# Performance work log

Measured on AMD Instinct MI355X. Metric: run time of the kernel, lower is better.

The kernel has to match this reference:

```python
import jax, jax.numpy as jnp
import numpy as np
from jax import lax

H = 8          # num_heads
LAM = 4.0      # lambda_scale
POOL = 8       # pool_ratio (effective, N % POOL == 0)
NS_ITERS = 5
NS_EPS = 1e-4
WHITE_EPS = 1e-5


def _lap_kernel(x, y):
    # x: [B,H,n,D], y: [B,H,m,D] -> exp(-||x_i - y_j||_1 / LAM): [B,H,n,m]
    l1 = jnp.sum(jnp.abs(x[:, :, :, None, :] - y[:, :, None, :, :]), axis=-1)
    return jnp.exp(-l1 / LAM)


def setup_inputs() -> dict:
    key = jax.random.key(0)
    ks = jax.random.split(key, 8)
    B, N, C = 2, 1024, 512
    s = 0.05  # weight scale for realistic magnitudes
    return {
        "x": jax.random.normal(ks[0], (B, N, C), jnp.float32),
        "attention_mask": jnp.ones((B, N), jnp.float32),
        "qkv_w": jax.random.normal(ks[1], (3 * C, C), jnp.float32) * s,
        "qkv_b": jax.random.normal(ks[2], (3 * C,), jnp.float32) * s,
        "proj_w": jax.random.normal(ks[3], (C, C), jnp.float32) * s,
        "proj_b": jax.random.normal(ks[4], (C,), jnp.float32) * s,
        "dwc_w": jax.random.normal(ks[5], (C, 1, 3), jnp.float32) * s,
        "dwc_b": jax.random.normal(ks[6], (C,), jnp.float32) * s,
    }


def reference(x, attention_mask, qkv_w, qkv_b, proj_w, proj_b, dwc_w, dwc_b):
    B, N, C = x.shape
    D = C // H
    tm = attention_mask                      # [B,N]
    mh = tm[:, None, :, None]                # [B,1,N,1] broadcast over heads

    qkv = (x @ qkv_w.T + qkv_b).reshape(B, N, 3, H, D).transpose(2, 0, 3, 1, 4)
    q, k, v = qkv[0] * mh, qkv[1] * mh, qkv[2] * mh   # [B,H,N,D]

    # NOTE: faithful to source: raw reshape of [B,N,H*D] into [B,C,N]
    v_sp = v.transpose(0, 2, 1, 3).reshape(B, C, N)
    q_sp = q.transpose(0, 2, 1, 3).reshape(B, C, N)
    k_sp = k.transpose(0, 2, 1, 3).reshape(B, C, N)

    # depthwise conv1d, kernel 3, padding 1
    v_local = lax.conv_general_dilated(
        v_sp, dwc_w, window_strides=(1,), padding=[(1, 1)],
        feature_group_count=C, dimension_numbers=("NCH", "OIH", "NCH")
    ) + dwc_b[None, :, None]
    v_local = v_local.transpose(0, 2, 1) * tm[:, :, None]   # [B,N,C]

    p = POOL
    m = N // p
    pm = tm.reshape(B, 1, m, p).mean(-1)                    # [B,1,m]
    pms = jnp.clip(pm, 1e-6)
    q_pool = (q_sp * tm[:, None, :]).reshape(B, C, m, p).mean(-1) / pms
    k_pool = (k_sp * tm[:, None, :]).reshape(B, C, m, p).mean(-1) / pms
    lmask = (pm > 0).astype(x.dtype)[:, 0, :]               # [B,m]

    q_l = q_pool.transpose(0, 2, 1).reshape(B, m, H, D).transpose(0, 2, 1, 3)
    k_l = k_pool.transpose(0, 2, 1).reshape(B, m, H, D).transpose(0, 2, 1, 3)

    W = _lap_kernel(q_l, k_l)                               # [B,H,m,m]
    pair = lmask[:, None, :, None] * lmask[:, None, None, :]
    I = jnp.eye(m, dtype=x.dtype)[None, None]
    W = W * pair + I * (1.0 - pair)

    # Newton-Schulz pseudo-inverse
    W_eps = W + NS_EPS * I
    fro = jnp.sqrt(jnp.sum(W_eps * W_eps, axis=(-2, -1), keepdims=True))
    X = (2.0 / (fro + 1e-8)) * jnp.swapaxes(W_eps, -2, -1)
    for _ in range(NS_ITERS):
        X = X @ (2.0 * I - W_eps @ X)
    W_inv = X

    la_mask = lmask[:, None, None, :]                        # [B,1,1,m]
    C_q = _lap_kernel(q, k_l) * la_mask                      # [B,H,N,m]
    C_k = _lap_kernel(k, q_l) * la_mask                      # [B,H,N,m]

    # batch-statistics whitening of C_q over dims (0,2)
    qmask = tm[:, None, :, None]                             # [B,1,N,1]
    valid = jnp.clip(jnp.sum(qmask, axis=(0, 2), keepdims=True), 1.0)
    mu = jnp.sum(C_q * qmask, axis=(0, 2), keepdims=True) / valid
    cen = (C_q - mu) * qmask
    var = jnp.sum(cen * cen, axis=(0, 2), keepdims=True) / valid
    C_q_norm = ((C_q - mu) / jnp.sqrt(var + WHITE_EPS)) * qmask

    context = W_inv @ (jnp.swapaxes(C_k, -2, -1) @ v)        # [B,H,m,D]
    ga = (C_q_norm @ context) * mh                           # [B,H,N,D]
    ga = ga.transpose(0, 2, 1, 3).reshape(B, N, C)

    out = (ga + v_local) @ proj_w.T + proj_b
    return out * tm[:, :, None]
```

## Files before the change

### kernel.cpp

```cpp
#include <hip/hip_runtime.h>
#include <hip/hip_bf16.h>
#include <hip/hip_fp16.h>

#define Hh 8
#define Bz 2
#define Nn 1024
#define Cc 512
#define Dd 64
#define Mm 128
#define NS_EPS 1e-4f
#define WHITE_EPS 1e-5f

__device__ __forceinline__ float h2f(__half v) { return __half2float(v); }
__device__ __forceinline__ __half f2h(float v) { return __float2half(v); }

typedef _Float16 half8 __attribute__((ext_vector_type(8)));
typedef float float4v __attribute__((ext_vector_type(4)));

__global__ __launch_bounds__(256) void qkv_gemm(
    const float* __restrict__ x, const float* __restrict__ w,
    const float* __restrict__ bias, const float* __restrict__ tm,
    __half* __restrict__ Q, __half* __restrict__ K, __half* __restrict__ V) {
  __shared__ _Float16 As[128 * 40];
  __shared__ _Float16 Bs[128 * 40];
// ... 90 lines not shown
    for (int i = 0; i < 8; ++i) {
      float t = tm[b * 1024 + 8 * j + i];
      pm += t;
      sq += Qs[d][8 * jl + i] * t;
      sk += Ks[d][8 * jl + i] * t;
    }
    pm *= 0.125f;
    float pms = fmaxf(pm, 1e-6f);
    size_t oi = ((size_t)bh * 128 + j) * 64 + d;
    QL[oi] = f2h(sq * 0.125f / pms);
    KL[oi] = f2h(sk * 0.125f / pms);
    if (h == 0 && d == 0) LM[b * 128 + j] = (pm > 0.f) ? 1.f : 0.f;
  }
}

__global__ __launch_bounds__(256) void wbuild_kernel(
    const __half* __restrict__ QL, const __half* __restrict__ KL,
    const float* __restrict__ LM, float* __restrict__ W) {
  int it = blockIdx.x;
  int bh = blockIdx.y;
  int b = bh >> 3;
  int i0 = it * 16;
  __shared__ __align__(16) float kls[128 * 68];
  __shared__ __align__(16) float qs[16 * 68];
  __shared__ float ps[16 * 132];
  int tid = threadIdx.x;
  for (int e = tid; e < 8192; e += 256)
    kls[(e >> 6) * 68 + (e & 63)] = h2f(KL[(size_t)bh * 8192 + e]);
  for (int e = tid; e < 1024; e += 256)
    qs[(e >> 6) * 68 + (e & 63)] =
        h2f(QL[(size_t)bh * 8192 + (size_t)(i0 + (e >> 6)) * 64 + (e & 63)]);
  __syncthreads();
  int jg = tid & 63, ng = tid >> 6;
  int j = jg * 2;
  const float4* kA = (const float4*)&kls[j * 68];
  const float4* kB = (const float4*)&kls[(j + 1) * 68];
  float sA[4] = {}, sB[4] = {};
#pragma unroll
  for (int i = 0; i < 16; ++i) {
    int dq = (i + jg) & 15;
    float4 ka = kA[dq];
    float4 kb = kB[dq];
#pragma unroll
    for (int r = 0; r < 4; ++r) {
      float4 qv = *(const float4*)&qs[(ng * 4 + r) * 68 + dq * 4];
      sA[r] += fabsf(qv.x - ka.x) + fabsf(qv.y - ka.y) + fabsf(qv.z - ka.z) + fabsf(qv.w - ka.w);
      sB[r] += fabsf(qv.x - kb.x) + fabsf(qv.y - kb.y) + fabsf(qv.z - kb.z) + fabsf(qv.w - kb.w);
    }
  }
  float lmA = LM[b * Mm + j], lmB = LM[b * Mm + j + 1];
#pragma unroll
  for (int r = 0; r < 4; ++r) {
    int i = i0 + ng * 4 + r;
    float lmi = LM[b * Mm + i];
    float prA = lmi * lmA, prB = lmi * lmB;
    float dA = (i == j) ? 1.f : 0.f;
    float dB = (i == j + 1) ? 1.f : 0.f;
    ps[(ng * 4 + r) * 132 + j] = expf(-sA[r] * 0.25f) * prA + dA * (1.f - prA) + dA * NS_EPS;
    ps[(ng * 4 + r) * 132 + j + 1] = expf(-sB[r] * 0.25f) * prB + dB * (1.f - prB) + dB * NS_EPS;
  }
  __syncthreads();
  for (int e = tid; e < 2048; e += 256)
    W[(size_t)bh * (Mm * Mm) + (size_t)(i0 + (e >> 7)) * 128 + (e & 127)] =
        ps[(e >> 7) * 132 + (e & 127)];
}

__global__ __launch_bounds__(256) void ns_solve(const float* __restrict__ Wg,
                                                float* __restrict__ Xout) {
  int bh = blockIdx.x;
  __shared__ _Float16 Ws[128 * 136];
  __shared__ _Float16 Xa[128 * 136];
  __shared__ _Float16 Xb[128 * 136];
  __shared__ _Float16 Tt[128 * 136];
  __shared__ float red[256];
  int tid = threadIdx.x;
  const float* Wb = Wg + (size_t)bh * 16384;
  float fro = 0.f;
  for (int e = tid; e < 16384; e += 256) {
    float wv = Wb[e];
    Ws[(e >> 7) * 136 + (e & 127)] = (_Float16)wv;
    fro += wv * wv;
  }
  red[tid] = fro;
  __syncthreads();
  for (int off = 128; off > 0; off >>= 1) {
    if (tid < off) red[tid] += red[tid + off];
    __syncthreads();
  }
  float scale = 2.f / (sqrtf(red[0]) + 1e-8f);
  for (int e = tid; e < 16384; e += 256) {
    int i = e >> 7, k = e & 127;
    Xa[i * 136 + k] = (_Float16)(scale * (float)Ws[k * 136 + i]);
    Xb[i * 136 + k] = (_Float16)(scale * (float)Ws[i * 136 + k]);
  }
  __syncthreads();
  int lane = tid & 63, wv_ = tid >> 6;
  int wm = (wv_ >> 1) * 64, wn = (wv_ & 1) * 64;
  int l15 = lane & 15, quad = lane >> 4;
  for (int it = 0; it < 5; ++it) {
    {
      float4v acc[4][4] = {};
#pragma unroll
      for (int kt = 0; kt < 4; ++kt) {
        half8 a[4], b[4];
#pragma unroll
        for (int mt = 0; mt < 4; ++mt)
          a[mt] = *(const half8*)&Ws[(wm + mt * 16 + l15) * 136 + kt * 32 + quad * 8];
#pragma unroll
        for (int nt = 0; nt < 4; ++nt)
          b[nt] = *(const half8*)&Xb[(wn + nt * 16 + l15) * 136 + kt * 32 + quad * 8];
#pragma unroll
        for (int mt = 0; mt < 4; ++mt)
#pragma unroll
          for (int nt = 0; nt < 4; ++nt)
            acc[mt][nt] =
                __builtin_amdgcn_mfma_f32_16x16x32_f16(a[mt], b[nt], acc[mt][nt], 0, 0, 0);
      }
#pragma unroll
      for (int mt = 0; mt < 4; ++mt)
#pragma unroll
        for (int r = 0; r < 4; ++r) {
          int i = wm + mt * 16 + quad * 4 + r;
#pragma unroll
          for (int nt = 0; nt < 4; ++nt) {
            int j = wn + nt * 16 + l15;
            Tt[j * 136 + i] = (_Float16)(((i == j) ? 2.f : 0.f) - acc[mt][nt][r]);
          }
        }
    }
    __syncthreads();
    {
      float4v acc[4][4] = {};
#pragma unroll
      for (int kt = 0; kt < 4; ++kt) {
        half8 a[4], b[4];
#pragma unroll
        for (int mt = 0; mt < 4; ++mt)
          a[mt] = *(const half8*)&Xa[(wm + mt * 16 + l15) * 136 + kt * 32 + quad * 8];
#pragma unroll
        for (int nt = 0; nt < 4; ++nt)
          b[nt] = *(const half8*)&Tt[(wn + nt * 16 + l15) * 136 + kt * 32 + quad * 8];
#pragma unroll
        for (int mt = 0; mt < 4; ++mt)
#pragma unroll
          for (int nt = 0; nt < 4; ++nt)
            acc[mt][nt] =
                __builtin_amdgcn_mfma_f32_16x16x32_f16(a[mt], b[nt], acc[mt][nt], 0, 0, 0);
      }
      __syncthreads();
#pragma unroll
      for (int mt = 0; mt < 4; ++mt)
#pragma unroll
        for (int r = 0; r < 4; ++r) {
          int i = wm + mt * 16 + quad * 4 + r;
#pragma unroll
          for (int nt = 0; nt < 4; ++nt) {
            int j = wn + nt * 16 + l15;
            _Float16 v = (_Float16)acc[mt][nt][r];
            Xa[i * 136 + j] = v;
            Xb[j * 136 + i] = v;
          }
        }
    }
    __syncthreads();
  }
  for (int e = tid; e < 16384; e += 256)
    Xout[(size_t)bh * 16384 + e] = (float)Xa[(e >> 7) * 136 + (e & 127)];
}

__global__ __launch_bounds__(256) void ktv_fused(
    const __half* __restrict__ K, const __half* __restrict__ QL,
    const float* __restrict__ LM, const __half* __restrict__ V,
    float* __restrict__ KTVp) {
  int jt = blockIdx.x;
  int bh = blockIdx.y;
  int nc = blockIdx.z;
  int b = bh >> 3, h = bh & 7;
  int j0 = jt * 32;
  __shared__ __align__(16) float qls[32 * 68];
  __shared__ __align__(16) float Ks[32 * 68];
  __shared__ __align__(16) float Vs[32 * 68];
  __shared__ float P[32 * 36];
  int tid = threadIdx.x;
  int sr = tid >> 3, sd8 = (tid & 7) * 8;
  {
    half8 q = *(const half8*)(QL + (size_t)bh * 8192 + (size_t)(j0 + sr) * 64 + sd8);
    float4 f0 = {(float)q[0], (float)q[1], (float)q[2], (float)q[3]};
    float4 f1 = {(float)q[4], (float)q[5], (float)q[6], (float)q[7]};
    *(float4*)&qls[sr * 68 + sd8] = f0;
    *(float4*)&qls[sr * 68 + sd8 + 4] = f1;
  }
  int jq = tid & 15, nq = tid >> 4;
  int dq2 = tid & 7, jl = tid >> 3;
  float acc[8] = {};
  for (int nt = 0; nt < 4; ++nt) {
    int n0 = nc * 128 + nt * 32;
    __syncthreads();
    {
      size_t gi = (size_t)b * (Nn * Cc) + (size_t)(n0 + sr) * 512 + h * 64 + sd8;
      half8 kv = *(const half8*)(K + gi);
      half8 vv = *(const half8*)(V + gi);
      float4 k0 = {(float)kv[0], (float)kv[1], (float)kv[2], (float)kv[3]};
      float4 k1 = {(float)kv[4], (float)kv[5], (float)kv[6], (float)kv[7]};
      float4 v0 = {(float)vv[0], (float)vv[1], (float)vv[2], (float)vv[3]};
      float4 v1 = {(float)vv[4], (float)vv[5], (float)vv[6], (float)vv[7]};
      *(float4*)&Ks[sr * 68 + sd8] = k0;
      *(float4*)&Ks[sr * 68 + sd8 + 4] = k1;
      *(float4*)&Vs[sr * 68 + sd8] = v0;
      *(float4*)&Vs[sr * 68 + sd8 + 4] = v1;
    }
    __syncthreads();
    {
      const float4* q0p = (const float4*)&qls[(jq * 2) * 68];
      const float4* q1p = (const float4*)&qls[(jq * 2 + 1) * 68];
      const float4* k0p = (const float4*)&Ks[(nq * 2) * 68];
      const float4* k1p = (const float4*)&Ks[(nq * 2 + 1) * 68];
      float s00 = 0.f, s01 = 0.f, s10 = 0.f, s11 = 0.f;
#pragma unroll
      for (int i = 0; i < 16; ++i) {
        int dq = (i + tid) & 15;
        float4 q0 = q0p[dq], q1 = q1p[dq];
        float4 k0 = k0p[dq], k1 = k1p[dq];
        s00 += fabsf(q0.x - k0.x) + fabsf(q0.y - k0.y) + fabsf(q0.z - k0.z) + fabsf(q0.w - k0.w);
        s01 += fabsf(q0.x - k1.x) + fabsf(q0.y - k1.y) + fabsf(q0.z - k1.z) + fabsf(q0.w - k1.w);
        s10 += fabsf(q1.x - k0.x) + fabsf(q1.y - k0.y) + fabsf(q1.z - k0.z) + fabsf(q1.w - k0.w);
        s11 += fabsf(q1.x - k1.x) + fabsf(q1.y - k1.y) + fabsf(q1.z - k1.z) + fabsf(q1.w - k1.w);
      }
      P[(nq * 2) * 36 + jq * 2] = expf(-s00 * 0.25f);
      P[(nq * 2) * 36 + jq * 2 + 1] = expf(-s10 * 0.25f);
      P[(nq * 2 + 1) * 36 + jq * 2] = expf(-s01 * 0.25f);
      P[(nq * 2 + 1) * 36 + jq * 2 + 1] = expf(-s11 * 0.25f);
    }
    __syncthreads();
    {
#pragma unroll 4
      for (int n = 0; n < 32; ++n) {
        float p = P[n * 36 + jl];
        float4 v0 = *(const float4*)&Vs[n * 68 + dq2 * 8];
        float4 v1 = *(const float4*)&Vs[n * 68 + dq2 * 8 + 4];
        acc[0] += p * v0.x; acc[1] += p * v0.y; acc[2] += p * v0.z; acc[3] += p * v0.w;
        acc[4] += p * v1.x; acc[5] += p * v1.y; acc[6] += p * v1.z; acc[7] += p * v1.w;
      }
    }
  }
  {
    float lm = LM[b * 128 + j0 + jl];
    float* dst = &KTVp[((size_t)nc * 16 + bh) * 8192 + (size_t)(j0 + jl) * 64 + dq2 * 8];
    float4 o0 = {acc[0] * lm, acc[1] * lm, acc[2] * lm, acc[3] * lm};
    float4 o1 = {acc[4] * lm, acc[5] * lm, acc[6] * lm, acc[7] * lm};
    *(float4*)dst = o0;
    *(float4*)(dst + 4) = o1;
  }
}

__global__ __launch_bounds__(256) void ctx_kernel(const float* __restrict__ X,
                                                  const float* __restrict__ KTVp,
                                                  __half* __restrict__ CTX) {
  int it = blockIdx.x;
  int bh = blockIdx.y;
  int i0 = it * 16;
  __shared__ __align__(16) float KTVs[8192];
  __shared__ float Xs[16][132];
  int tid = threadIdx.x;
  const float4* src = (const float4*)KTVp;
  for (int e = tid; e < 2048; e += 256) {
    float4 s = src[(size_t)bh * 2048 + e];
#pragma unroll
    for (int nc = 1; nc < 8; ++nc) {
      float4 v = src[((size_t)nc * 16 + bh) * 2048 + e];
      s.x += v.x; s.y += v.y; s.z += v.z; s.w += v.w;
    }
    *(float4*)&KTVs[e * 4] = s;
  }
  for (int e = tid; e < 2048; e += 256)
    Xs[e >> 7][e & 127] = X[(size_t)bh * 16384 + (size_t)(i0 + (e >> 7)) * 128 + (e & 127)];
  __syncthreads();
  int il = tid >> 4, dg = tid & 15;
  float a0 = 0.f, a1 = 0.f, a2 = 0.f, a3 = 0.f;
#pragma unroll 4
  for (int j = 0; j < 128; ++j) {
    float xv = Xs[il][j];
    float4 kv = *(const float4*)&KTVs[j * 64 + dg * 4];
    a0 += xv * kv.x; a1 += xv * kv.y; a2 += xv * kv.z; a3 += xv * kv.w;
  }
  size_t ob = (size_t)bh * 8192 + (size_t)(i0 + il) * 64 + dg * 4;
  CTX[ob] = f2h(a0);
  CTX[ob + 1] = f2h(a1);
  CTX[ob + 2] = f2h(a2);
  CTX[ob + 3] = f2h(a3);
}

__global__ __launch_bounds__(256) void stats_partial(
    const __half* __restrict__ Q, const __half* __restrict__ KL,
    const float* __restrict__ LM, const float* __restrict__ tm,
    float* __restrict__ PS, __half* __restrict__ Pbuf) {
  int jt = blockIdx.x;
  int bh = blockIdx.y;
  int nc = blockIdx.z;
  int b = bh >> 3, h = bh & 7;
  int j0 = jt * 32;
  __shared__ __align__(16) float kls[32 * 68];
  __shared__ __align__(16) float Qs[32 * 68];
  __shared__ float red[32 * 8 * 3];
  int tid = threadIdx.x;
  int sr = tid >> 3, sd8 = (tid & 7) * 8;
  {
    half8 q = *(const half8*)(KL + (size_t)bh * 8192 + (size_t)(j0 + sr) * 64 + sd8);
    float4 f0 = {(float)q[0], (float)q[1], (float)q[2], (float)q[3]};
    float4 f1 = {(float)q[4], (float)q[5], (float)q[6], (float)q[7]};
    *(float4*)&kls[sr * 68 + sd8] = f0;
    *(float4*)&kls[sr * 68 + sd8 + 4] = f1;
  }
  int jq = tid & 15, nq = tid >> 4;
  int jA = j0 + jq * 2, jB = jA + 1;
  float lmA = LM[b * 128 + jA], lmB = LM[b * 128 + jB];
  float aA1 = 0.f, aA2 = 0.f, aA3 = 0.f, aB1 = 0.f, aB2 = 0.f, aB3 = 0.f;
  for (int nt = 0; nt < 4; ++nt) {
    int n0 = nc * 128 + nt * 32;
    __syncthreads();
    {
      size_t gi = (size_t)b * (Nn * Cc) + (size_t)(n0 + sr) * 512 + h * 64 + sd8;
      half8 kv = *(const half8*)(Q + gi);
      float4 k0 = {(float)kv[0], (float)kv[1], (float)kv[2], (float)kv[3]};
      float4 k1 = {(float)kv[4], (float)kv[5], (float)kv[6], (float)kv[7]};
      *(float4*)&Qs[sr * 68 + sd8] = k0;
      *(float4*)&Qs[sr * 68 + sd8 + 4] = k1;
    }
    __syncthreads();
    const float4* q0p = (const float4*)&kls[(jq * 2) * 68];
    const float4* q1p = (const float4*)&kls[(jq * 2 + 1) * 68];
    const float4* k0p = (const float4*)&Qs[(nq * 2) * 68];
    const float4* k1p = (const float4*)&Qs[(nq * 2 + 1) * 68];
    float s00 = 0.f, s01 = 0.f, s10 = 0.f, s11 = 0.f;
#pragma unroll
    for (int i = 0; i < 16; ++i) {
      int dq = (i + tid) & 15;
      float4 q0 = q0p[dq], q1 = q1p[dq];
      float4 k0 = k0p[dq], k1 = k1p[dq];
      s00 += fabsf(q0.x - k0.x) + fabsf(q0.y - k0.y) + fabsf(q0.z - k0.z) + fabsf(q0.w - k0.w);
      s01 += fabsf(q0.x - k1.x) + fabsf(q0.y - k1.y) + fabsf(q0.z - k1.z) + fabsf(q0.w - k1.w);
      s10 += fabsf(q1.x - k0.x) + fabsf(q1.y - k0.y) + fabsf(q1.z - k0.z) + fabsf(q1.w - k0.w);
      s11 += fabsf(q1.x - k1.x) + fabsf(q1.y - k1.y) + fabsf(q1.z - k1.z) + fabsf(q1.w - k1.w);
    }
    int nA = n0 + nq * 2, nB = nA + 1;
    float tA = tm[b * 1024 + nA], tB = tm[b * 1024 + nB];
    float xAa = expf(-s00 * 0.25f) * lmA;
    float xAb = expf(-s01 * 0.25f) * lmA;
    float xBa = expf(-s10 * 0.25f) * lmB;
    float xBb = expf(-s11 * 0.25f) * lmB;
    Pbuf[((size_t)bh * 1024 + nA) * 128 + jA] = f2h(xAa);
    Pbuf[((size_t)bh * 1024 + nB) * 128 + jA] = f2h(xAb);
    Pbuf[((size_t)bh * 1024 + nA) * 128 + jB] = f2h(xBa);
    Pbuf[((size_t)bh * 1024 + nB) * 128 + jB] = f2h(xBb);
    float xt;
    xt = xAa * tA; aA1 += xt; aA2 += xt * xt; aA3 += xt * tA;
    xt = xAb * tB; aA1 += xt; aA2 += xt * xt; aA3 += xt * tB;
    xt = xBa * tA; aB1 += xt; aB2 += xt * xt; aB3 += xt * tA;
    xt = xBb * tB; aB1 += xt; aB2 += xt * xt; aB3 += xt * tB;
  }
  int jl = jq * 2;
  red[(jl * 8 + nq) * 3 + 0] = aA1;
  red[(jl * 8 + nq) * 3 + 1] = aA2;
  red[(jl * 8 + nq) * 3 + 2] = aA3;
  red[((jl + 1) * 8 + nq) * 3 + 0] = aB1;
  red[((jl + 1) * 8 + nq) * 3 + 1] = aB2;
  red[((jl + 1) * 8 + nq) * 3 + 2] = aB3;
  __syncthreads();
  if (tid < 32) {
    float s1 = 0.f, s2 = 0.f, s3 = 0.f;
#pragma unroll
    for (int q = 0; q < 8; ++q) {
      s1 += red[(tid * 8 + q) * 3 + 0];
      s2 += red[(tid * 8 + q) * 3 + 1];
      s3 += red[(tid * 8 + q) * 3 + 2];
    }
    size_t base = ((size_t)(nc * 16 + bh) * 128 + j0 + tid) * 3;
    PS[base] = s1; PS[base + 1] = s2; PS[base + 2] = s3;
  }
}

__global__ __launch_bounds__(256) void stats_final(const float* __restrict__ PS,
                                                   const float* __restrict__ tm,
                                                   float* __restrict__ MU,
                                                   float* __restrict__ RS) {
  __shared__ float red[256][2];
  __shared__ float ts0, ts1;
  int tid = threadIdx.x;
  float a = 0.f, c = 0.f;
  for (int i = tid; i < 2048; i += 256) { float t = tm[i]; a += t; c += t * t; }
  red[tid][0] = a; red[tid][1] = c;
  __syncthreads();
  for (int off = 128; off > 0; off >>= 1) {
    if (tid < off) { red[tid][0] += red[tid + off][0]; red[tid][1] += red[tid + off][1]; }
    __syncthreads();
  }
  if (tid == 0) { ts0 = red[0][0]; ts1 = red[0][1]; }
  __syncthreads();
  int hj = blockIdx.x * 256 + tid;
  int h = hj >> 7, j = hj & 127;
  float s1 = 0.f, s2 = 0.f, s3 = 0.f;
#pragma unroll
  for (int nc = 0; nc < 8; ++nc)
#pragma unroll
    for (int b = 0; b < 2; ++b) {
      const float* p = PS + ((size_t)(nc * 16 + b * 8 + h) * 128 + j) * 3;
      s1 += p[0]; s2 += p[1]; s3 += p[2];
    }
  float valid = fmaxf(ts0, 1.f);
  float mu = s1 / valid;
  float var = (s2 - 2.f * mu * s3 + mu * mu * ts1) / valid;
  var = fmaxf(var, 0.f);
  MU[hj] = mu;
  RS[hj] = rsqrtf(var + WHITE_EPS);
}

__global__ __launch_bounds__(256) void ga_fused(
    const __half* __restrict__ Pbuf, const float* __restrict__ MU,
    const float* __restrict__ RS, const __half* __restrict__ CTXg,
    const __half* __restrict__ V, const float* __restrict__ dwc_w,
    const float* __restrict__ dwc_b, const float* __restrict__ tm,
    __half* __restrict__ VL) {
  int bh = blockIdx.y;
  int b = bh >> 3, h = bh & 7;
  int n0 = blockIdx.x * 16;
  __shared__ __half Ps[16][130];
  __shared__ __align__(16) __half2 ctx2[128][32];
  __shared__ float musr[128][2];
  int tid = threadIdx.x;
// ... 106 lines not shown
                              void* d_out, int out_size, void* d_ws, size_t ws_size,
                              hipStream_t stream) {
  const float* x      = (const float*)d_in[0];
  const float* tm     = (const float*)d_in[1];
  const float* qkv_w  = (const float*)d_in[2];
  const float* qkv_b  = (const float*)d_in[3];
  const float* proj_w = (const float*)d_in[4];
  const float* proj_b = (const float*)d_in[5];
  const float* dwc_w  = (const float*)d_in[6];
  const float* dwc_b  = (const float*)d_in[7];
  float* out = (float*)d_out;

  char* wsb = (char*)d_ws;
  __half* Qh  = (__half*)(wsb + 0);
  __half* Kh  = (__half*)(wsb + 2097152);
  __half* Vh  = (__half*)(wsb + 4194304);
  __half* VLh = (__half*)(wsb + 6291456);
  __half* QLh = (__half*)(wsb + 8388608);
  __half* KLh = (__half*)(wsb + 8650752);
  float*  LM  = (float*)(wsb + 8912896);
  float*  MU  = (float*)(wsb + 8913920);
  float*  RS  = (float*)(wsb + 8918016);
  __half* CTX = (__half*)(wsb + 9446400);
  float*  XA  = (float*)(wsb + 9708544);
  float*  PS  = (float*)(wsb + 9708544 + 1048576);

  char* ob = (char*)d_out;
  float*  Wf   = (float*)ob;
  float*  KTVp = (float*)ob;
  __half* Pbuf = (__half*)ob;

  qkv_gemm<<<dim3(16, 12), 256, 0, stream>>>(x, qkv_w, qkv_b, tm, Qh, Kh, Vh);
  pool_kernel<<<dim3(16, 16), 256, 0, stream>>>(Qh, Kh, tm, QLh, KLh, LM);
  wbuild_kernel<<<dim3(8, 16), 256, 0, stream>>>(QLh, KLh, LM, Wf);
  ns_solve<<<16, 256, 0, stream>>>(Wf, XA);
  ktv_fused<<<dim3(4, 16, 8), 256, 0, stream>>>(Kh, QLh, LM, Vh, KTVp);
  ctx_kernel<<<dim3(8, 16), 256, 0, stream>>>(XA, KTVp, CTX);
  stats_partial<<<dim3(4, 16, 8), 256, 0, stream>>>(Qh, KLh, LM, tm, PS, Pbuf);
  stats_final<<<4, 256, 0, stream>>>(PS, tm, MU, RS);
  ga_fused<<<dim3(64, 16), 256, 0, stream>>>(Pbuf, MU, RS, CTX, Vh, dwc_w, dwc_b, tm, VLh);
  proj_gemm<<<dim3(16, 4), 256, 0, stream>>>(VLh, proj_w, proj_b, tm, out);
}
```

Measured before the change: 236.4 us.

## Merge independent mid-pipeline kernels into two heterogeneous fused launches

```diff
diff --git a/kernel.cpp b/kernel.cpp
--- a/kernel.cpp
+++ b/kernel.cpp
@@ -128,207 +128,51 @@
   }
 }
 
-__global__ __launch_bounds__(256) void wbuild_kernel(
-    const __half* __restrict__ QL, const __half* __restrict__ KL,
-    const float* __restrict__ LM, float* __restrict__ W) {
-  int it = blockIdx.x;
-  int bh = blockIdx.y;
-  int b = bh >> 3;
-  int i0 = it * 16;
-  __shared__ __align__(16) float kls[128 * 68];
-  __shared__ __align__(16) float qs[16 * 68];
-  __shared__ float ps[16 * 132];
+__global__ __launch_bounds__(256) void fused_phase1(
+    const __half* __restrict__ Q, const __half* __restrict__ K,
+    const __half* __restrict__ V, const __half* __restrict__ QL,
+    const __half* __restrict__ KL, const float* __restrict__ LM,
+    const float* __restrict__ tm, __half* __restrict__ Wh,
+    float* __restrict__ KTVp, float* __restrict__ PS,
+    __half* __restrict__ Pbuf) {
+  __shared__ __align__(16) char smem[47616];
+  int id = blockIdx.x;
   int tid = threadIdx.x;
-  for (int e = tid; e < 8192; e += 256)
-    kls[(e >> 6) * 68 + (e & 63)] = h2f(KL[(size_t)bh * 8192 + e]);
-  for (int e = tid; e < 1024; e += 256)
-    qs[(e >> 6) * 68 + (e & 63)] =
-        h2f(QL[(size_t)bh * 8192 + (size_t)(i0 + (e >> 6)) * 64 + (e & 63)]);
-  __syncthreads();
-  int jg = tid & 63, ng = tid >> 6;
-  int j = jg * 2;
-  const float4* kA = (const float4*)&kls[j * 68];
-  const float4* kB = (const float4*)&kls[(j + 1) * 68];
-  float sA[4] = {}, sB[4] = {};
-#pragma unroll
-  for (int i = 0; i < 16; ++i) {
-    int dq = (i + jg) & 15;
-    float4 ka = kA[dq];
-    float4 kb = kB[dq];
-#pragma unroll
-    for (int r = 0; r < 4; ++r) {
-      float4 qv = *(const float4*)&qs[(ng * 4 + r) * 68 + dq * 4];
-      sA[r] += fabsf(qv.x - ka.x) + fabsf(qv.y - ka.y) + fabsf(qv.z - ka.z) + fabsf(qv.w - ka.w);
-      sB[r] += fabsf(qv.x - kb.x) + fabsf(qv.y - kb.y) + fabsf(qv.z - kb.z) + fabsf(qv.w - kb.w);
-    }
-  }
-  float lmA = LM[b * Mm + j], lmB = LM[b * Mm + j + 1];
-#pragma unroll
-  for (int r = 0; r < 4; ++r) {
-    int i = i0 + ng * 4 + r;
-    float lmi = LM[b * Mm + i];
-    float prA = lmi * lmA, prB = lmi * lmB;
-    float dA = (i == j) ? 1.f : 0.f;
-    float dB = (i == j + 1) ? 1.f : 0.f;
-    ps[(ng * 4 + r) * 132 + j] = expf(-sA[r] * 0.25f) * prA + dA * (1.f - prA) + dA * NS_EPS;
-    ps[(ng * 4 + r) * 132 + j + 1] = expf(-sB[r] * 0.25f) * prB + dB * (1.f - prB) + dB * NS_EPS;
-  }
-  __syncthreads();
-  for (int e = tid; e < 2048; e += 256)
-    W[(size_t)bh * (Mm * Mm) + (size_t)(i0 + (e >> 7)) * 128 + (e & 127)] =
-        ps[(e >> 7) * 132 + (e & 127)];
-}
-
-__global__ __launch_bounds__(256) void ns_solve(const float* __restrict__ Wg,
-                                                float* __restrict__ Xout) {
-  int bh = blockIdx.x;
-  __shared__ _Float16 Ws[128 * 136];
-  __shared__ _Float16 Xa[128 * 136];
-  __shared__ _Float16 Xb[128 * 136];
-  __shared__ _Float16 Tt[128 * 136];
-  __shared__ float red[256];
-  int tid = threadIdx.x;
-  const float* Wb = Wg + (size_t)bh * 16384;
-  float fro = 0.f;
-  for (int e = tid; e < 16384; e += 256) {
-    float wv = Wb[e];
-    Ws[(e >> 7) * 136 + (e & 127)] = (_Float16)wv;
-    fro += wv * wv;
-  }
-  red[tid] = fro;
-  __syncthreads();
-  for (int off = 128; off > 0; off >>= 1) {
-    if (tid < off) red[tid] += red[tid + off];
-    __syncthreads();
-  }
-  float scale = 2.f / (sqrtf(red[0]) + 1e-8f);
-  for (int e = tid; e < 16384; e += 256) {
-    int i = e >> 7, k = e & 127;
-    Xa[i * 136 + k] = (_Float16)(scale * (float)Ws[k * 136 + i]);
-    Xb[i * 136 + k] = (_Float16)(scale * (float)Ws[i * 136 + k]);
-  }
-  __syncthreads();
-  int lane = tid & 63, wv_ = tid >> 6;
-  int wm = (wv_ >> 1) * 64, wn = (wv_ & 1) * 64;
-  int l15 = lane & 15, quad = lane >> 4;
-  for (int it = 0; it < 5; ++it) {
+  if (id < 512) {
+    int jt = id & 3, bh = (id >> 2) & 15, nc = id >> 6;
+    int b = bh >> 3, h = bh & 7;
+    int j0 = jt * 32;
+    float* kls = (float*)smem;
+    float* Qs = (float*)(smem + 8704);
+    float* red = (float*)(smem + 17408);
+    int sr = tid >> 3, sd8 = (tid & 7) * 8;
     {
-      float4v acc[4][4] = {};
-#pragma unroll
-      for (int kt = 0; kt < 4; ++kt) {
-        half8 a[4], b[4];
-#pragma unroll
-        for (int mt = 0; mt < 4; ++mt)
-          a[mt] = *(const half8*)&Ws[(wm + mt * 16 + l15) * 136 + kt * 32 + quad * 8];
-#pragma unroll
-        for (int nt = 0; nt < 4; ++nt)
-          b[nt] = *(const half8*)&Xb[(wn + nt * 16 + l15) * 136 + kt * 32 + quad * 8];
-#pragma unroll
-        for (int mt = 0; mt < 4; ++mt)
-#pragma unroll
-          for (int nt = 0; nt < 4; ++nt)
-            acc[mt][nt] =
-                __builtin_amdgcn_mfma_f32_16x16x32_f16(a[mt], b[nt], acc[mt][nt], 0, 0, 0);
-      }
-#pragma unroll
-      for (int mt = 0; mt < 4; ++mt)
-#pragma unroll
-        for (int r = 0; r < 4; ++r) {
-          int i = wm + mt * 16 + quad * 4 + r;
-#pragma unroll
-          for (int nt = 0; nt < 4; ++nt) {
-            int j = wn + nt * 16 + l15;
-            Tt[j * 136 + i] = (_Float16)(((i == j) ? 2.f : 0.f) - acc[mt][nt][r]);
-          }
-        }
-    }
-    __syncthreads();
-    {
-      float4v acc[4][4] = {};
-#pragma unroll
-      for (int kt = 0; kt < 4; ++kt) {
-        half8 a[4], b[4];
-#pragma unroll
-        for (int mt = 0; mt < 4; ++mt)
-          a[mt] = *(const half8*)&Xa[(wm + mt * 16 + l15) * 136 + kt * 32 + quad * 8];
-#pragma unroll
-        for (int nt = 0; nt < 4; ++nt)
-          b[nt] = *(const half8*)&Tt[(wn + nt * 16 + l15) * 136 + kt * 32 + quad * 8];
-#pragma unroll
-        for (int mt = 0; mt < 4; ++mt)
-#pragma unroll
-          for (int nt = 0; nt < 4; ++nt)
-            acc[mt][nt] =
-                __builtin_amdgcn_mfma_f32_16x16x32_f16(a[mt], b[nt], acc[mt][nt], 0, 0, 0);
-      }
-      __syncthreads();
-#pragma unroll
-      for (int mt = 0; mt < 4; ++mt)
-#pragma unroll
-        for (int r = 0; r < 4; ++r) {
-          int i = wm + mt * 16 + quad * 4 + r;
-#pragma unroll
-          for (int nt = 0; nt < 4; ++nt) {
-            int j = wn + nt * 16 + l15;
-            _Float16 v = (_Float16)acc[mt][nt][r];
-            Xa[i * 136 + j] = v;
-            Xb[j * 136 + i] = v;
-          }
-        }
-    }
-    __syncthreads();
-  }
-  for (int e = tid; e < 16384; e += 256)
-    Xout[(size_t)bh * 16384 + e] = (float)Xa[(e >> 7) * 136 + (e & 127)];
-}
-
-__global__ __launch_bounds__(256) void ktv_fused(
-    const __half* __restrict__ K, const __half* __restrict__ QL,
-    const float* __restrict__ LM, const __half* __restrict__ V,
-    float* __restrict__ KTVp) {
-  int jt = blockIdx.x;
-  int bh = blockIdx.y;
-  int nc = blockIdx.z;
-  int b = bh >> 3, h = bh & 7;
-  int j0 = jt * 32;
-  __shared__ __align__(16) float qls[32 * 68];
-  __shared__ __align__(16) float Ks[32 * 68];
-  __shared__ __align__(16) float Vs[32 * 68];
-  __shared__ float P[32 * 36];
-  int tid = threadIdx.x;
-  int sr = tid >> 3, sd8 = (tid & 7) * 8;
-  {
-    half8 q = *(const half8*)(QL + (size_t)bh * 8192 + (size_t)(j0 + sr) * 64 + sd8);
-    float4 f0 = {(float)q[0], (float)q[1], (float)q[2], (float)q[3]};
-    float4 f1 = {(float)q[4], (float)q[5], (float)q[6], (float)q[7]};
-    *(float4*)&qls[sr * 68 + sd8] = f0;
-    *(float4*)&qls[sr * 68 + sd8 + 4] = f1;
-  }
-  int jq = tid & 15, nq = tid >> 4;
-  int dq2 = tid & 7, jl = tid >> 3;
-  float acc[8] = {};
-  for (int nt = 0; nt < 4; ++nt) {
-    int n0 = nc * 128 + nt * 32;
-    __syncthreads();
-    {
-      size_t gi = (size_t)b * (Nn * Cc) + (size_t)(n0 + sr) * 512 + h * 64 + sd8;
-      half8 kv = *(const half8*)(K + gi);
-      half8 vv = *(const half8*)(V + gi);
-      float4 k0 = {(float)kv[0], (float)kv[1], (float)kv[2], (float)kv[3]};
-      float4 k1 = {(float)kv[4], (float)kv[5], (float)kv[6], (float)kv[7]};
-      float4 v0 = {(float)vv[0], (float)vv[1], (float)vv[2], (float)vv[3]};
-      float4 v1 = {(float)vv[4], (float)vv[5], (float)vv[6], (float)vv[7]};
-      *(float4*)&Ks[sr * 68 + sd8] = k0;
-      *(float4*)&Ks[sr * 68 + sd8 + 4] = k1;
-      *(float4*)&Vs[sr * 68 + sd8] = v0;
-      *(float4*)&Vs[sr * 68 + sd8 + 4] = v1;
-    }
-    __syncthreads();
-    {
-      const float4* q0p = (const float4*)&qls[(jq * 2) * 68];
-      const float4* q1p = (const float4*)&qls[(jq * 2 + 1) * 68];
-      const float4* k0p = (const float4*)&Ks[(nq * 2) * 68];
-      const float4* k1p = (const float4*)&Ks[(nq * 2 + 1) * 68];
+      half8 q = *(const half8*)(KL + (size_t)bh * 8192 + (size_t)(j0 + sr) * 64 + sd8);
+      float4 f0 = {(float)q[0], (float)q[1], (float)q[2], (float)q[3]};
+      float4 f1 = {(float)q[4], (float)q[5], (float)q[6], (float)q[7]};
+      *(float4*)&kls[sr * 68 + sd8] = f0;
+      *(float4*)&kls[sr * 68 + sd8 + 4] = f1;
+    }
+    int jq = tid & 15, nq = tid >> 4;
+    int jA = j0 + jq * 2, jB = jA + 1;
+    float lmA = LM[b * 128 + jA], lmB = LM[b * 128 + jB];
+    float aA1 = 0.f, aA2 = 0.f, aA3 = 0.f, aB1 = 0.f, aB2 = 0.f, aB3 = 0.f;
+    for (int nt = 0; nt < 4; ++nt) {
+      int n0 = nc * 128 + nt * 32;
+      __syncthreads();
+      {
+        size_t gi = (size_t)b * (Nn * Cc) + (size_t)(n0 + sr) * 512 + h * 64 + sd8;
+        half8 kv = *(const half8*)(Q + gi);
+        float4 k0 = {(float)kv[0], (float)kv[1], (float)kv[2], (float)kv[3]};
+        float4 k1 = {(float)kv[4], (float)kv[5], (float)kv[6], (float)kv[7]};
+        *(float4*)&Qs[sr * 68 + sd8] = k0;
+        *(float4*)&Qs[sr * 68 + sd8 + 4] = k1;
+      }
+      __syncthreads();
+      const float4* q0p = (const float4*)&kls[(jq * 2) * 68];
+      const float4* q1p = (const float4*)&kls[(jq * 2 + 1) * 68];
+      const float4* k0p = (const float4*)&Qs[(nq * 2) * 68];
+      const float4* k1p = (const float4*)&Qs[(nq * 2 + 1) * 68];
       float s00 = 0.f, s01 = 0.f, s10 = 0.f, s11 = 0.f;
 #pragma unroll
       for (int i = 0; i < 16; ++i) {
@@ -340,30 +184,302 @@
         s10 += fabsf(q1.x - k0.x) + fabsf(q1.y - k0.y) + fabsf(q1.z - k0.z) + fabsf(q1.w - k0.w);
         s11 += fabsf(q1.x - k1.x) + fabsf(q1.y - k1.y) + fabsf(q1.z - k1.z) + fabsf(q1.w - k1.w);
       }
-      P[(nq * 2) * 36 + jq * 2] = expf(-s00 * 0.25f);
-      P[(nq * 2) * 36 + jq * 2 + 1] = expf(-s10 * 0.25f);
-      P[(nq * 2 + 1) * 36 + jq * 2] = expf(-s01 * 0.25f);
-      P[(nq * 2 + 1) * 36 + jq * 2 + 1] = expf(-s11 * 0.25f);
-    }
-    __syncthreads();
+      int nA = n0 + nq * 2, nB = nA + 1;
+      float tA = tm[b * 1024 + nA], tB = tm[b * 1024 + nB];
+      float xAa = expf(-s00 * 0.25f) * lmA;
+      float xAb = expf(-s01 * 0.25f) * lmA;
+      float xBa = expf(-s10 * 0.25f) * lmB;
+      float xBb = expf(-s11 * 0.25f) * lmB;
+      Pbuf[((size_t)bh * 1024 + nA) * 128 + jA] = f2h(xAa);
+      Pbuf[((size_t)bh * 1024 + nB) * 128 + jA] = f2h(xAb);
+      Pbuf[((size_t)bh * 1024 + nA) * 128 + jB] = f2h(xBa);
+      Pbuf[((size_t)bh * 1024 + nB) * 128 + jB] = f2h(xBb);
+      float xt;
+      xt = xAa * tA; aA1 += xt; aA2 += xt * xt; aA3 += xt * tA;
+      xt = xAb * tB; aA1 += xt; aA2 += xt * xt; aA3 += xt * tB;
+      xt = xBa * tA; aB1 += xt; aB2 += xt * xt; aB3 += xt * tA;
+      xt = xBb * tB; aB1 += xt; aB2 += xt * xt; aB3 += xt * tB;
+    }
+    int jl = jq * 2;
+    red[(jl * 8 + nq) * 3 + 0] = aA1;
+    red[(jl * 8 + nq) * 3 + 1] = aA2;
+    red[(jl * 8 + nq) * 3 + 2] = aA3;
+    red[((jl + 1) * 8 + nq) * 3 + 0] = aB1;
+    red[((jl + 1) * 8 + nq) * 3 + 1] = aB2;
+    red[((jl + 1) * 8 + nq) * 3 + 2] = aB3;
+    __syncthreads();
+    if (tid < 32) {
+      float s1 = 0.f, s2 = 0.f, s3 = 0.f;
+#pragma unroll
+      for (int q = 0; q < 8; ++q) {
+        s1 += red[(tid * 8 + q) * 3 + 0];
+        s2 += red[(tid * 8 + q) * 3 + 1];
+        s3 += red[(tid * 8 + q) * 3 + 2];
+      }
+      size_t base = ((size_t)(nc * 16 + bh) * 128 + j0 + tid) * 3;
+      PS[base] = s1; PS[base + 1] = s2; PS[base + 2] = s3;
+    }
+  } else if (id < 768) {
+    int kid = id - 512;
+    int jt = kid & 3, bh = (kid >> 2) & 15, nc = kid >> 6;
+    int b = bh >> 3, h = bh & 7;
+    int j0 = jt * 32;
+    float* qls = (float*)smem;
+    float* Ks = (float*)(smem + 8704);
+    float* Vs = (float*)(smem + 17408);
+    float* P = (float*)(smem + 26112);
+    int sr = tid >> 3, sd8 = (tid & 7) * 8;
     {
+      half8 q = *(const half8*)(QL + (size_t)bh * 8192 + (size_t)(j0 + sr) * 64 + sd8);
+      float4 f0 = {(float)q[0], (float)q[1], (float)q[2], (float)q[3]};
+      float4 f1 = {(float)q[4], (float)q[5], (float)q[6], (float)q[7]};
+      *(float4*)&qls[sr * 68 + sd8] = f0;
+      *(float4*)&qls[sr * 68 + sd8 + 4] = f1;
+    }
+    int jq = tid & 15, nq = tid >> 4;
+    int dq2 = tid & 7, jl = tid >> 3;
+    float acc[8] = {};
+    for (int nt = 0; nt < 8; ++nt) {
+      int n0 = nc * 256 + nt * 32;
+      __syncthreads();
+      {
+        size_t gi = (size_t)b * (Nn * Cc) + (size_t)(n0 + sr) * 512 + h * 64 + sd8;
+        half8 kv = *(const half8*)(K + gi);
+        half8 vv = *(const half8*)(V + gi);
+        float4 k0 = {(float)kv[0], (float)kv[1], (float)kv[2], (float)kv[3]};
+        float4 k1 = {(float)kv[4], (float)kv[5], (float)kv[6], (float)kv[7]};
+        float4 v0 = {(float)vv[0], (float)vv[1], (float)vv[2], (float)vv[3]};
+        float4 v1 = {(float)vv[4], (float)vv[5], (float)vv[6], (float)vv[7]};
+        *(float4*)&Ks[sr * 68 + sd8] = k0;
+        *(float4*)&Ks[sr * 68 + sd8 + 4] = k1;
+        *(float4*)&Vs[sr * 68 + sd8] = v0;
+        *(float4*)&Vs[sr * 68 + sd8 + 4] = v1;
+      }
+      __syncthreads();
+      {
+        const float4* q0p = (const float4*)&qls[(jq * 2) * 68];
+        const float4* q1p = (const float4*)&qls[(jq * 2 + 1) * 68];
+        const float4* k0p = (const float4*)&Ks[(nq * 2) * 68];
+        const float4* k1p = (const float4*)&Ks[(nq * 2 + 1) * 68];
+        float s00 = 0.f, s01 = 0.f, s10 = 0.f, s11 = 0.f;
+#pragma unroll
+        for (int i = 0; i < 16; ++i) {
+          int dq = (i + tid) & 15;
+          float4 q0 = q0p[dq], q1 = q1p[dq];
+          float4 k0 = k0p[dq], k1 = k1p[dq];
+          s00 += fabsf(q0.x - k0.x) + fabsf(q0.y - k0.y) + fabsf(q0.z - k0.z) + fabsf(q0.w - k0.w);
+          s01 += fabsf(q0.x - k1.x) + fabsf(q0.y - k1.y) + fabsf(q0.z - k1.z) + fabsf(q0.w - k1.w);
+          s10 += fabsf(q1.x - k0.x) + fabsf(q1.y - k0.y) + fabsf(q1.z - k0.z) + fabsf(q1.w - k0.w);
+          s11 += fabsf(q1.x - k1.x) + fabsf(q1.y - k1.y) + fabsf(q1.z - k1.z) + fabsf(q1.w - k1.w);
+        }
+        P[(nq * 2) * 36 + jq * 2] = expf(-s00 * 0.25f);
+        P[(nq * 2) * 36 + jq * 2 + 1] = expf(-s10 * 0.25f);
+        P[(nq * 2 + 1) * 36 + jq * 2] = expf(-s01 * 0.25f);
+        P[(nq * 2 + 1) * 36 + jq * 2 + 1] = expf(-s11 * 0.25f);
+      }
+      __syncthreads();
+      {
 #pragma unroll 4
-      for (int n = 0; n < 32; ++n) {
-        float p = P[n * 36 + jl];
-        float4 v0 = *(const float4*)&Vs[n * 68 + dq2 * 8];
-        float4 v1 = *(const float4*)&Vs[n * 68 + dq2 * 8 + 4];
-        acc[0] += p * v0.x; acc[1] += p * v0.y; acc[2] += p * v0.z; acc[3] += p * v0.w;
-        acc[4] += p * v1.x; acc[5] += p * v1.y; acc[6] += p * v1.z; acc[7] += p * v1.w;
-      }
-    }
-  }
-  {
-    float lm = LM[b * 128 + j0 + jl];
-    float* dst = &KTVp[((size_t)nc * 16 + bh) * 8192 + (size_t)(j0 + jl) * 64 + dq2 * 8];
-    float4 o0 = {acc[0] * lm, acc[1] * lm, acc[2] * lm, acc[3] * lm};
-    float4 o1 = {acc[4] * lm, acc[5] * lm, acc[6] * lm, acc[7] * lm};
-    *(float4*)dst = o0;
-    *(float4*)(dst + 4) = o1;
+        for (int n = 0; n < 32; ++n) {
+          float p = P[n * 36 + jl];
+          float4 v0 = *(const float4*)&Vs[n * 68 + dq2 * 8];
+          float4 v1 = *(const float4*)&Vs[n * 68 + dq2 * 8 + 4];
+          acc[0] += p * v0.x; acc[1] += p * v0.y; acc[2] += p * v0.z; acc[3] += p * v0.w;
+          acc[4] += p * v1.x; acc[5] += p * v1.y; acc[6] += p * v1.z; acc[7] += p * v1.w;
+        }
+      }
+    }
+    {
+      float lm = LM[b * 128 + j0 + jl];
+      float* dst = &KTVp[((size_t)nc * 16 + bh) * 8192 + (size_t)(j0 + jl) * 64 + dq2 * 8];
+      float4 o0 = {acc[0] * lm, acc[1] * lm, acc[2] * lm, acc[3] * lm};
+      float4 o1 = {acc[4] * lm, acc[5] * lm, acc[6] * lm, acc[7] * lm};
+      *(float4*)dst = o0;
+      *(float4*)(dst + 4) = o1;
+    }
+  } else {
+    int wid = id - 768;
+    int it = wid >> 4, bh = wid & 15;
+    int b = bh >> 3;
+    int i0 = it * 16;
+    float* kls = (float*)smem;
+    float* qs = (float*)(smem + 34816);
+    float* ps = (float*)(smem + 39168);
+    for (int e = tid; e < 8192; e += 256)
+      kls[(e >> 6) * 68 + (e & 63)] = h2f(KL[(size_t)bh * 8192 + e]);
+    for (int e = tid; e < 1024; e += 256)
+      qs[(e >> 6) * 68 + (e & 63)] =
+          h2f(QL[(size_t)bh * 8192 + (size_t)(i0 + (e >> 6)) * 64 + (e & 63)]);
+    __syncthreads();
+    int jg = tid & 63, ng = tid >> 6;
+    int j = jg * 2;
+    const float4* kA = (const float4*)&kls[j * 68];
+    const float4* kB = (const float4*)&kls[(j + 1) * 68];
+    float sA[4] = {}, sB[4] = {};
+#pragma unroll
+    for (int i = 0; i < 16; ++i) {
+      int dq = (i + jg) & 15;
+      float4 ka = kA[dq];
+      float4 kb = kB[dq];
+#pragma unroll
+      for (int r = 0; r < 4; ++r) {
+        float4 qv = *(const float4*)&qs[(ng * 4 + r) * 68 + dq * 4];
+        sA[r] += fabsf(qv.x - ka.x) + fabsf(qv.y - ka.y) + fabsf(qv.z - ka.z) + fabsf(qv.w - ka.w);
+        sB[r] += fabsf(qv.x - kb.x) + fabsf(qv.y - kb.y) + fabsf(qv.z - kb.z) + fabsf(qv.w - kb.w);
+      }
+    }
+    float lmA = LM[b * Mm + j], lmB = LM[b * Mm + j + 1];
+#pragma unroll
+    for (int r = 0; r < 4; ++r) {
+      int i = i0 + ng * 4 + r;
+      float lmi = LM[b * Mm + i];
+      float prA = lmi * lmA, prB = lmi * lmB;
+      float dA = (i == j) ? 1.f : 0.f;
+      float dB = (i == j + 1) ? 1.f : 0.f;
+      ps[(ng * 4 + r) * 132 + j] = expf(-sA[r] * 0.25f) * prA + dA * (1.f - prA) + dA * NS_EPS;
+      ps[(ng * 4 + r) * 132 + j + 1] = expf(-sB[r] * 0.25f) * prB + dB * (1.f - prB) + dB * NS_EPS;
+    }
+    __syncthreads();
+    for (int e = tid; e < 2048; e += 256)
+      Wh[(size_t)bh * (Mm * Mm) + (size_t)(i0 + (e >> 7)) * 128 + (e & 127)] =
+          f2h(ps[(e >> 7) * 132 + (e & 127)]);
+  }
+}
+
+__global__ __launch_bounds__(256) void fused_phase2(
+    const __half* __restrict__ Wh, float* __restrict__ Xout,
+    const float* __restrict__ PS, const float* __restrict__ tm,
+    float* __restrict__ MU, float* __restrict__ RS) {
+  __shared__ __align__(16) char smem[140288];
+  int tid = threadIdx.x;
+  if (blockIdx.x < 16) {
+    int bh = blockIdx.x;
+    _Float16* Ws = (_Float16*)smem;
+    _Float16* Xa = (_Float16*)(smem + 34816);
+    _Float16* Xb = (_Float16*)(smem + 69632);
+    _Float16* Tt = (_Float16*)(smem + 104448);
+    float* red = (float*)(smem + 139264);
+    const __half* Wb = Wh + (size_t)bh * 16384;
+    float fro = 0.f;
+    for (int e = tid; e < 16384; e += 256) {
+      float wv = h2f(Wb[e]);
+      Ws[(e >> 7) * 136 + (e & 127)] = (_Float16)wv;
+      fro += wv * wv;
+    }
+    red[tid] = fro;
+    __syncthreads();
+    for (int off = 128; off > 0; off >>= 1) {
+      if (tid < off) red[tid] += red[tid + off];
+      __syncthreads();
+    }
+    float scale = 2.f / (sqrtf(red[0]) + 1e-8f);
+    for (int e = tid; e < 16384; e += 256) {
+      int i = e >> 7, k = e & 127;
+      Xa[i * 136 + k] = (_Float16)(scale * (float)Ws[k * 136 + i]);
+      Xb[i * 136 + k] = (_Float16)(scale * (float)Ws[i * 136 + k]);
+    }
+    __syncthreads();
+    int lane = tid & 63, wv_ = tid >> 6;
+    int wm = (wv_ >> 1) * 64, wn = (wv_ & 1) * 64;
+    int l15 = lane & 15, quad = lane >> 4;
+    for (int it = 0; it < 5; ++it) {
+      {
+        float4v acc[4][4] = {};
+#pragma unroll
+        for (int kt = 0; kt < 4; ++kt) {
+          half8 a[4], b[4];
+#pragma unroll
+          for (int mt = 0; mt < 4; ++mt)
+            a[mt] = *(const half8*)&Ws[(wm + mt * 16 + l15) * 136 + kt * 32 + quad * 8];
+#pragma unroll
+          for (int nt = 0; nt < 4; ++nt)
+            b[nt] = *(const half8*)&Xb[(wn + nt * 16 + l15) * 136 + kt * 32 + quad * 8];
+#pragma unroll
+          for (int mt = 0; mt < 4; ++mt)
+#pragma unroll
+            for (int nt = 0; nt < 4; ++nt)
+              acc[mt][nt] =
+                  __builtin_amdgcn_mfma_f32_16x16x32_f16(a[mt], b[nt], acc[mt][nt], 0, 0, 0);
+        }
+#pragma unroll
+        for (int mt = 0; mt < 4; ++mt)
+#pragma unroll
+          for (int r = 0; r < 4; ++r) {
+            int i = wm + mt * 16 + quad * 4 + r;
+#pragma unroll
+            for (int nt = 0; nt < 4; ++nt) {
+              int j = wn + nt * 16 + l15;
+              Tt[j * 136 + i] = (_Float16)(((i == j) ? 2.f : 0.f) - acc[mt][nt][r]);
+            }
+          }
+      }
+      __syncthreads();
+      {
+        float4v acc[4][4] = {};
+#pragma unroll
+        for (int kt = 0; kt < 4; ++kt) {
+          half8 a[4], b[4];
+#pragma unroll
+          for (int mt = 0; mt < 4; ++mt)
+            a[mt] = *(const half8*)&Xa[(wm + mt * 16 + l15) * 136 + kt * 32 + quad * 8];
+#pragma unroll
+          for (int nt = 0; nt < 4; ++nt)
+            b[nt] = *(const half8*)&Tt[(wn + nt * 16 + l15) * 136 + kt * 32 + quad * 8];
+#pragma unroll
+          for (int mt = 0; mt < 4; ++mt)
+#pragma unroll
+            for (int nt = 0; nt < 4; ++nt)
+              acc[mt][nt] =
+                  __builtin_amdgcn_mfma_f32_16x16x32_f16(a[mt], b[nt], acc[mt][nt], 0, 0, 0);
+        }
+        __syncthreads();
+#pragma unroll
+        for (int mt = 0; mt < 4; ++mt)
+#pragma unroll
+          for (int r = 0; r < 4; ++r) {
+            int i = wm + mt * 16 + quad * 4 + r;
+#pragma unroll
+            for (int nt = 0; nt < 4; ++nt) {
+              int j = wn + nt * 16 + l15;
+              _Float16 v = (_Float16)acc[mt][nt][r];
+              Xa[i * 136 + j] = v;
+              Xb[j * 136 + i] = v;
+            }
+          }
+      }
+      __syncthreads();
+    }
+    for (int e = tid; e < 16384; e += 256)
+      Xout[(size_t)bh * 16384 + e] = (float)Xa[(e >> 7) * 136 + (e & 127)];
+  } else {
+    float (*red2)[2] = (float(*)[2])smem;
+    float* ts = (float*)(smem + 2048);
+    float a = 0.f, c = 0.f;
+    for (int i = tid; i < 2048; i += 256) { float t = tm[i]; a += t; c += t * t; }
+    red2[tid][0] = a; red2[tid][1] = c;
+    __syncthreads();
+    for (int off = 128; off > 0; off >>= 1) {
+      if (tid < off) { red2[tid][0] += red2[tid + off][0]; red2[tid][1] += red2[tid + off][1]; }
+      __syncthreads();
+    }
+    if (tid == 0) { ts[0] = red2[0][0]; ts[1] = red2[0][1]; }
+    __syncthreads();
+    int hj = (blockIdx.x - 16) * 256 + tid;
+    int h = hj >> 7, j = hj & 127;
+    float s1 = 0.f, s2 = 0.f, s3 = 0.f;
+#pragma unroll
+    for (int nc = 0; nc < 8; ++nc)
+#pragma unroll
+      for (int b = 0; b < 2; ++b) {
+        const float* p = PS + ((size_t)(nc * 16 + b * 8 + h) * 128 + j) * 3;
+        s1 += p[0]; s2 += p[1]; s3 += p[2];
+      }
+    float valid = fmaxf(ts[0], 1.f);
+    float mu = s1 / valid;
+    float var = (s2 - 2.f * mu * s3 + mu * mu * ts[1]) / valid;
+    var = fmaxf(var, 0.f);
+    MU[hj] = mu;
+    RS[hj] = rsqrtf(var + WHITE_EPS);
   }
 }
 
@@ -380,7 +496,7 @@
   for (int e = tid; e < 2048; e += 256) {
     float4 s = src[(size_t)bh * 2048 + e];
 #pragma unroll
-    for (int nc = 1; nc < 8; ++nc) {
+    for (int nc = 1; nc < 4; ++nc) {
       float4 v = src[((size_t)nc * 16 + bh) * 2048 + e];
       s.x += v.x; s.y += v.y; s.z += v.z; s.w += v.w;
     }
@@ -402,130 +518,6 @@
   CTX[ob + 1] = f2h(a1);
   CTX[ob + 2] = f2h(a2);
   CTX[ob + 3] = f2h(a3);
-}
-
-__global__ __launch_bounds__(256) void stats_partial(
-    const __half* __restrict__ Q, const __half* __restrict__ KL,
-    const float* __restrict__ LM, const float* __restrict__ tm,
-    float* __restrict__ PS, __half* __restrict__ Pbuf) {
-  int jt = blockIdx.x;
-  int bh = blockIdx.y;
-  int nc = blockIdx.z;
-  int b = bh >> 3, h = bh & 7;
-  int j0 = jt * 32;
-  __shared__ __align__(16) float kls[32 * 68];
-  __shared__ __align__(16) float Qs[32 * 68];
-  __shared__ float red[32 * 8 * 3];
-  int tid = threadIdx.x;
-  int sr = tid >> 3, sd8 = (tid & 7) * 8;
-  {
-    half8 q = *(const half8*)(KL + (size_t)bh * 8192 + (size_t)(j0 + sr) * 64 + sd8);
-    float4 f0 = {(float)q[0], (float)q[1], (float)q[2], (float)q[3]};
-    float4 f1 = {(float)q[4], (float)q[5], (float)q[6], (float)q[7]};
-    *(float4*)&kls[sr * 68 + sd8] = f0;
-    *(float4*)&kls[sr * 68 + sd8 + 4] = f1;
-  }
-  int jq = tid & 15, nq = tid >> 4;
-  int jA = j0 + jq * 2, jB = jA + 1;
-  float lmA = LM[b * 128 + jA], lmB = LM[b * 128 + jB];
-  float aA1 = 0.f, aA2 = 0.f, aA3 = 0.f, aB1 = 0.f, aB2 = 0.f, aB3 = 0.f;
-  for (int nt = 0; nt < 4; ++nt) {
-    int n0 = nc * 128 + nt * 32;
-    __syncthreads();
-    {
-      size_t gi = (size_t)b * (Nn * Cc) + (size_t)(n0 + sr) * 512 + h * 64 + sd8;
-      half8 kv = *(const half8*)(Q + gi);
-      float4 k0 = {(float)kv[0], (float)kv[1], (float)kv[2], (float)kv[3]};
-      float4 k1 = {(float)kv[4], (float)kv[5], (float)kv[6], (float)kv[7]};
-      *(float4*)&Qs[sr * 68 + sd8] = k0;
-      *(float4*)&Qs[sr * 68 + sd8 + 4] = k1;
-    }
-    __syncthreads();
-    const float4* q0p = (const float4*)&kls[(jq * 2) * 68];
-    const float4* q1p = (const float4*)&kls[(jq * 2 + 1) * 68];
-    const float4* k0p = (const float4*)&Qs[(nq * 2) * 68];
-    const float4* k1p = (const float4*)&Qs[(nq * 2 + 1) * 68];
-    float s00 = 0.f, s01 = 0.f, s10 = 0.f, s11 = 0.f;
-#pragma unroll
-    for (int i = 0; i < 16; ++i) {
-      int dq = (i + tid) & 15;
-      float4 q0 = q0p[dq], q1 = q1p[dq];
-      float4 k0 = k0p[dq], k1 = k1p[dq];
-      s00 += fabsf(q0.x - k0.x) + fabsf(q0.y - k0.y) + fabsf(q0.z - k0.z) + fabsf(q0.w - k0.w);
-      s01 += fabsf(q0.x - k1.x) + fabsf(q0.y - k1.y) + fabsf(q0.z - k1.z) + fabsf(q0.w - k1.w);
-      s10 += fabsf(q1.x - k0.x) + fabsf(q1.y - k0.y) + fabsf(q1.z - k0.z) + fabsf(q1.w - k0.w);
-      s11 += fabsf(q1.x - k1.x) + fabsf(q1.y - k1.y) + fabsf(q1.z - k1.z) + fabsf(q1.w - k1.w);
-    }
-    int nA = n0 + nq * 2, nB = nA + 1;
-    float tA = tm[b * 1024 + nA], tB = tm[b * 1024 + nB];
-    float xAa = expf(-s00 * 0.25f) * lmA;
-    float xAb = expf(-s01 * 0.25f) * lmA;
-    float xBa = expf(-s10 * 0.25f) * lmB;
-    float xBb = expf(-s11 * 0.25f) * lmB;
-    Pbuf[((size_t)bh * 1024 + nA) * 128 + jA] = f2h(xAa);
-    Pbuf[((size_t)bh * 1024 + nB) * 128 + jA] = f2h(xAb);
-    Pbuf[((size_t)bh * 1024 + nA) * 128 + jB] = f2h(xBa);
-    Pbuf[((size_t)bh * 1024 + nB) * 128 + jB] = f2h(xBb);
-    float xt;
-    xt = xAa * tA; aA1 += xt; aA2 += xt * xt; aA3 += xt * tA;
-    xt = xAb * tB; aA1 += xt; aA2 += xt * xt; aA3 += xt * tB;
-    xt = xBa * tA; aB1 += xt; aB2 += xt * xt; aB3 += xt * tA;
-    xt = xBb * tB; aB1 += xt; aB2 += xt * xt; aB3 += xt * tB;
-  }
-  int jl = jq * 2;
-  red[(jl * 8 + nq) * 3 + 0] = aA1;
-  red[(jl * 8 + nq) * 3 + 1] = aA2;
-  red[(jl * 8 + nq) * 3 + 2] = aA3;
-  red[((jl + 1) * 8 + nq) * 3 + 0] = aB1;
-  red[((jl + 1) * 8 + nq) * 3 + 1] = aB2;
-  red[((jl + 1) * 8 + nq) * 3 + 2] = aB3;
-  __syncthreads();
-  if (tid < 32) {
-    float s1 = 0.f, s2 = 0.f, s3 = 0.f;
-#pragma unroll
-    for (int q = 0; q < 8; ++q) {
-      s1 += red[(tid * 8 + q) * 3 + 0];
-      s2 += red[(tid * 8 + q) * 3 + 1];
-      s3 += red[(tid * 8 + q) * 3 + 2];
-    }
-    size_t base = ((size_t)(nc * 16 + bh) * 128 + j0 + tid) * 3;
-    PS[base] = s1; PS[base + 1] = s2; PS[base + 2] = s3;
-  }
-}
-
-__global__ __launch_bounds__(256) void stats_final(const float* __restrict__ PS,
-                                                   const float* __restrict__ tm,
-                                                   float* __restrict__ MU,
-                                                   float* __restrict__ RS) {
-  __shared__ float red[256][2];
-  __shared__ float ts0, ts1;
-  int tid = threadIdx.x;
-  float a = 0.f, c = 0.f;
-  for (int i = tid; i < 2048; i += 256) { float t = tm[i]; a += t; c += t * t; }
-  red[tid][0] = a; red[tid][1] = c;
-  __syncthreads();
-  for (int off = 128; off > 0; off >>= 1) {
-    if (tid < off) { red[tid][0] += red[tid + off][0]; red[tid][1] += red[tid + off][1]; }
-    __syncthreads();
-  }
-  if (tid == 0) { ts0 = red[0][0]; ts1 = red[0][1]; }
-  __syncthreads();
-  int hj = blockIdx.x * 256 + tid;
-  int h = hj >> 7, j = hj & 127;
-  float s1 = 0.f, s2 = 0.f, s3 = 0.f;
-#pragma unroll
-  for (int nc = 0; nc < 8; ++nc)
-#pragma unroll
-    for (int b = 0; b < 2; ++b) {
-      const float* p = PS + ((size_t)(nc * 16 + b * 8 + h) * 128 + j) * 3;
-      s1 += p[0]; s2 += p[1]; s3 += p[2];
-    }
-  float valid = fmaxf(ts0, 1.f);
-  float mu = s1 / valid;
-  float var = (s2 - 2.f * mu * s3 + mu * mu * ts1) / valid;
-  var = fmaxf(var, 0.f);
-  MU[hj] = mu;
-  RS[hj] = rsqrtf(var + WHITE_EPS);
 }
 
 __global__ __launch_bounds__(256) void ga_fused(
@@ -662,30 +654,27 @@
   char* wsb = (char*)d_ws;
   __half* Qh  = (__half*)(wsb + 0);
   __half* Kh  = (__half*)(wsb + 2097152);
+  float*  XA  = (float*)(wsb + 2097152);
   __half* Vh  = (__half*)(wsb + 4194304);
   __half* VLh = (__half*)(wsb + 6291456);
+  float*  KTVp = (float*)(wsb + 6291456);
   __half* QLh = (__half*)(wsb + 8388608);
   __half* KLh = (__half*)(wsb + 8650752);
   float*  LM  = (float*)(wsb + 8912896);
   float*  MU  = (float*)(wsb + 8913920);
   float*  RS  = (float*)(wsb + 8918016);
-  __half* CTX = (__half*)(wsb + 9446400);
-  float*  XA  = (float*)(wsb + 9708544);
-  float*  PS  = (float*)(wsb + 9708544 + 1048576);
-
-  char* ob = (char*)d_out;
-  float*  Wf   = (float*)ob;
-  float*  KTVp = (float*)ob;
-  __half* Pbuf = (__half*)ob;
+  __half* CTX = (__half*)(wsb + 8922112);
+  float*  PS  = (float*)(wsb + 9184256);
+  __half* Wh  = (__half*)(wsb + 9380864);
+
+  __half* Pbuf = (__half*)d_out;
 
   qkv_gemm<<<dim3(16, 12), 256, 0, stream>>>(x, qkv_w, qkv_b, tm, Qh, Kh, Vh);
   pool_kernel<<<dim3(16, 16), 256, 0, stream>>>(Qh, Kh, tm, QLh, KLh, LM);
-  wbuild_kernel<<<dim3(8, 16), 256, 0, stream>>>(QLh, KLh, LM, Wf);
-  ns_solve<<<16, 256, 0, stream>>>(Wf, XA);
-  ktv_fused<<<dim3(4, 16, 8), 256, 0, stream>>>(Kh, QLh, LM, Vh, KTVp);
+  fused_phase1<<<896, 256, 0, stream>>>(Qh, Kh, Vh, QLh, KLh, LM, tm, Wh, KTVp,
+                                        PS, Pbuf);
+  fused_phase2<<<20, 256, 0, stream>>>(Wh, XA, PS, tm, MU, RS);
   ctx_kernel<<<dim3(8, 16), 256, 0, stream>>>(XA, KTVp, CTX);
-  stats_partial<<<dim3(4, 16, 8), 256, 0, stream>>>(Qh, KLh, LM, tm, PS, Pbuf);
-  stats_final<<<4, 256, 0, stream>>>(PS, tm, MU, RS);
   ga_fused<<<dim3(64, 16), 256, 0, stream>>>(Pbuf, MU, RS, CTX, Vh, dwc_w, dwc_b, tm, VLh);
   proj_gemm<<<dim3(16, 4), 256, 0, stream>>>(VLh, proj_w, proj_b, tm, out);
 }
```

New measurement: 219.1 us. 1.08x faster.
